# Kernel tuning notes

Hardware: AMD Instinct MI355X
Metric: run time of the kernel (lower is better)

Reference implementation:

```python
import jax, jax.numpy as jnp
import numpy as np

B, T, S, F, D, M = 8, 8192, 8192, 64, 64, 128
EPS = 1e-9


def _draw_omega(n_omega, d_feature, rng):
    # Stacked orthogonal blocks scaled by sqrt(d_feature), as in the TF module.
    n_blocks = (n_omega + d_feature - 1) // d_feature + 1
    blocks = []
    for _ in range(n_blocks):
        g = rng.standard_normal((d_feature, d_feature)).astype(np.float32)
        q, _ = np.linalg.qr(g)
        blocks.append(q * np.sqrt(float(d_feature)))
    return jnp.asarray(np.concatenate(blocks, axis=0)[:n_omega])


def setup_inputs() -> dict:
    k0 = jax.random.key(0)
    kq, kv, kk = jax.random.split(k0, 3)
    query = jax.random.normal(kq, (B, T, F), dtype=jnp.float32)
    value = jax.random.normal(kv, (B, S, D), dtype=jnp.float32)
    key = jax.random.normal(kk, (B, S, F), dtype=jnp.float32)
    omega = _draw_omega(M, F, np.random.default_rng(0))  # (M, F)
    return {"query": query, "value": value, "key": key, "omega": omega}


def _phi(x, omega):
    # x: (B, L, F) -> (B, L, 2M) positive random features
    m = omega.shape[0]
    square_sum = jnp.sum(x * x, axis=-1, keepdims=True) / 2.0  # (B, L, 1)
    xw = jnp.einsum('blf,mf->blm', x, omega)                   # (B, L, M)
    unnorm = jnp.exp(jnp.concatenate([xw, -xw], axis=-1) - square_sum) + EPS
    return unnorm / jnp.sqrt(2.0 * m)


def reference(query, value, key, omega):
    q = _phi(query, omega)  # (B, T, 2M)
    k = _phi(key, omega)    # (B, S, 2M)
    ones = jnp.ones(value.shape[:-1] + (1,), dtype=value.dtype)
    v1 = jnp.concatenate([value, ones], axis=-1)               # (B, S, D+1)
    kv = jnp.einsum('bsm,bsd->bmd', k, v1)                     # (B, 2M, D+1)
    qkv = jnp.einsum('btm,bmd->btd', q, kv)                    # (B, T, D+1)
    normalizer = qkv[:, :, -1:]
    return qkv[:, :, :-1] / normalizer
```

## Files before the change

kernel.cpp:

```cpp
#include <hip/hip_runtime.h>


constexpr int NB = 8;
constexpr int NT = 8192;
constexpr float EPSF = 1e-9f;
constexpr float SCALE = 0.0625f;

typedef short s8v __attribute__((ext_vector_type(8)));
typedef short s4v __attribute__((ext_vector_type(4)));
typedef float f4v __attribute__((ext_vector_type(4)));

__device__ inline f4v mfma16(s8v a, s8v b, f4v c) {
  return __builtin_amdgcn_mfma_f32_16x16x32_bf16(a, b, c, 0, 0, 0);
}

__device__ inline short bf16_rne(float f) {
  unsigned u = __builtin_bit_cast(unsigned, f);
  u += 0x7fffu + ((u >> 16) & 1u);
  return (short)(u >> 16);
}
__device__ inline float bf16_to_f(short h) {
  unsigned u = ((unsigned)(unsigned short)h) << 16;
  return __builtin_bit_cast(float, u);
}

__global__ void setup_omega(const float* __restrict__ omega,
                            short* __restrict__ ohf, short* __restrict__ olf) {
  int i = blockIdx.x * 256 + threadIdx.x;
  if (i >= 128 * 64) return;
  int jj = i & 7;
  int lane = (i >> 3) & 63;
  int h = (i >> 9) & 1;
  int ft = i >> 10;
  int m = ft * 16 + (lane & 15);
  int f = h * 32 + (lane >> 4) * 8 + jj;
  float wv = omega[m * 64 + f];
  short hh = bf16_rne(wv);
  ohf[i] = hh;
  olf[i] = bf16_rne(wv - bf16_to_f(hh));
}

struct PhiRows {
  s8v ah0, al0, ah1, al1;
  float ssr[4];
  float ss;
};

__device__ inline void split8(f4v a, f4v b, s8v& h, s8v& l) {
  float v[8] = {a.x, a.y, a.z, a.w, b.x, b.y, b.z, b.w};
#pragma unroll
  for (int j = 0; j < 8; ++j) {
    short hh = bf16_rne(v[j]);
    h[j] = hh;
    l[j] = bf16_rne(v[j] - bf16_to_f(hh));
  }
}

__device__ inline void load_phi_rows(const float* __restrict__ xrow_base, int lane, PhiRows& P) {
  const int r = lane & 15, q = lane >> 4;
  const float* p = xrow_base + r * 64 + q * 8;
  f4v u0 = *(const f4v*)(p);
  f4v u1 = *(const f4v*)(p + 4);
  f4v u2 = *(const f4v*)(p + 32);
  f4v u3 = *(const f4v*)(p + 36);
  float ss = u0.x * u0.x + u0.y * u0.y + u0.z * u0.z + u0.w * u0.w
           + u1.x * u1.x + u1.y * u1.y + u1.z * u1.z + u1.w * u1.w
           + u2.x * u2.x + u2.y * u2.y + u2.z * u2.z + u2.w * u2.w
           + u3.x * u3.x + u3.y * u3.y + u3.z * u3.z + u3.w * u3.w;
  ss += __shfl_xor(ss, 16, 64);
  ss += __shfl_xor(ss, 32, 64);
  ss *= 0.5f;
  P.ss = ss;
#pragma unroll
  for (int reg = 0; reg < 4; ++reg) P.ssr[reg] = __shfl(ss, q * 4 + reg, 64);
  split8(u0, u1, P.ah0, P.al0);
  split8(u2, u3, P.ah1, P.al1);
}

__device__ inline f4v phi_xw_tile(const PhiRows& P, const short* __restrict__ ohf,
                                  const short* __restrict__ olf, int ft, int lane) {
  const int o0 = ft * 1024 + lane * 8;
  s8v bh0 = *(const s8v*)(ohf + o0);
  s8v bh1 = *(const s8v*)(ohf + o0 + 512);
  s8v bl0 = *(const s8v*)(olf + o0);
  s8v bl1 = *(const s8v*)(olf + o0 + 512);
  f4v c = {0.f, 0.f, 0.f, 0.f};
  c = mfma16(P.ah0, bh0, c);
  c = mfma16(P.ah1, bh1, c);
  c = mfma16(P.al0, bh0, c);
  c = mfma16(P.al1, bh1, c);
  c = mfma16(P.ah0, bl0, c);
  c = mfma16(P.ah1, bl1, c);
  return c;
}

__device__ inline f4v phi_xw_tile_T(const PhiRows& P, const short* __restrict__ ohf,
                                    const short* __restrict__ olf, int ft, int lane) {
  const int o0 = ft * 1024 + lane * 8;
  s8v ah0 = *(const s8v*)(ohf + o0);
  s8v ah1 = *(const s8v*)(ohf + o0 + 512);
  s8v al0 = *(const s8v*)(olf + o0);
  s8v al1 = *(const s8v*)(olf + o0 + 512);
  f4v c = {0.f, 0.f, 0.f, 0.f};
  c = mfma16(ah0, P.ah0, c);
  c = mfma16(ah1, P.ah1, c);
  c = mfma16(al0, P.ah0, c);
  c = mfma16(al1, P.ah1, c);
  c = mfma16(ah0, P.al0, c);
  c = mfma16(ah1, P.al1, c);
  return c;
}

constexpr int KF_P = 72;
constexpr int QF_P = 264;
constexpr int PART_P = 72;
constexpr int PART_SZ = 256 * PART_P;

__global__ __launch_bounds__(256, 2) void kv_fused(
    const float* __restrict__ key, const float* __restrict__ value,
    const short* __restrict__ ohf, const short* __restrict__ olf,
    short* __restrict__ partial, float* __restrict__ kvacc, int use_partial) {
  __shared__ short kft[4 * 64 * KF_P];
  const int tid = threadIdx.x, lane = tid & 63, w = tid >> 6;
  const int b = blockIdx.x >> 6;
  const int s0 = (blockIdx.x & 63) * 128;
  const int q = lane >> 4, r15 = lane & 15;
  const int sign = w >> 1, th = w & 1;
  short* kw = kft + w * 64 * KF_P;

  s8v vone;
#pragma unroll
  for (int jj = 0; jj < 8; ++jj) vone[jj] = (r15 == 0) ? (short)0x3F80 : (short)0;

  f4v acc[4][5];
#pragma unroll
  for (int j = 0; j < 4; ++j)
#pragma unroll
    for (int n = 0; n < 5; ++n) acc[j][n] = f4v{0.f, 0.f, 0.f, 0.f};

  for (int sc = 0; sc < 2; ++sc) {
    const int sbase = s0 + sc * 64;
#pragma unroll
    for (int rg = 0; rg < 4; ++rg) {
      PhiRows P;
      load_phi_rows(key + ((size_t)b * NT + sbase + rg * 16) * 64, lane, P);
#pragma unroll
      for (int j = 0; j < 4; ++j) {
        f4v c = phi_xw_tile(P, ohf, olf, th * 4 + j, lane);
        s4v pk;
#pragma unroll
        for (int reg = 0; reg < 4; ++reg) {
          float xw = c[reg];
          float arg = sign ? (-xw - P.ssr[reg]) : (xw - P.ssr[reg]);
          pk[reg] = bf16_rne((__expf(arg) + EPSF) * SCALE);
        }
        *(s4v*)(kw + (j * 16 + r15) * KF_P + rg * 16 + q * 4) = pk;
      }
    }
    const float* vb = value + ((size_t)b * NT + sbase) * 64;
#pragma unroll
    for (int ks = 0; ks < 2; ++ks) {
      s8v bf[5];
#pragma unroll
      for (int n = 0; n < 4; ++n) {
#pragma unroll
        for (int jj = 0; jj < 8; ++jj)
          bf[n][jj] = bf16_rne(vb[(ks * 32 + q * 8 + jj) * 64 + n * 16 + r15]);
      }
      bf[4] = vone;
#pragma unroll
      for (int j = 0; j < 4; ++j) {
        s8v a = *(const s8v*)(kw + (j * 16 + r15) * KF_P + ks * 32 + q * 8);
#pragma unroll
        for (int n = 0; n < 5; ++n) acc[j][n] = mfma16(a, bf[n], acc[j][n]);
      }
    }
  }
  if (use_partial) {
#pragma unroll
    for (int j = 0; j < 4; ++j) {
#pragma unroll
      for (int n = 0; n < 4; ++n) {
#pragma unroll
        for (int reg = 0; reg < 4; ++reg)
          kw[(j * 16 + q * 4 + reg) * KF_P + n * 16 + r15] = bf16_rne(acc[j][n][reg]);
      }
      if (r15 == 0) {
#pragma unroll
        for (int reg = 0; reg < 4; ++reg)
          kw[(j * 16 + q * 4 + reg) * KF_P + 64] = bf16_rne(acc[j][4][reg]);
      }
    }
    short* pb = partial + (size_t)blockIdx.x * PART_SZ + w * 64 * PART_P;
#pragma unroll
    for (int i = 0; i < 9; ++i) {
      int e = i * 64 + lane;
      *(s8v*)(pb + e * 8) = *(const s8v*)(kw + e * 8);
    }
  } else {
    float* pb = kvacc + (size_t)b * PART_SZ;
#pragma unroll
    for (int j = 0; j < 4; ++j) {
      int m = w * 64 + j * 16 + q * 4;
#pragma unroll
      for (int n = 0; n < 4; ++n) {
        int d = n * 16 + r15;
#pragma unroll
        for (int reg = 0; reg < 4; ++reg)
          atomicAdd(pb + (size_t)(m + reg) * PART_P + d, acc[j][n][reg]);
      }
      if (r15 == 0)
#pragma unroll
        for (int reg = 0; reg < 4; ++reg)
          atomicAdd(pb + (size_t)(m + reg) * PART_P + 64, acc[j][4][reg]);
    }
  }
}

__global__ __launch_bounds__(256) void kv_finalize(
    const short* __restrict__ partial, const float* __restrict__ kvacc,
    short* __restrict__ kvfrag, int use_partial) {
  int i = blockIdx.x * 256 + threadIdx.x;
  int b = i / 20480;
  int rem = i - b * 20480;
  int m = rem / 80;
  int d = rem - m * 80;
  float s = 0.f;
  if (d < 65) {
    if (use_partial) {
      const short* p = partial + (size_t)(b * 64) * PART_SZ + m * PART_P + d;
#pragma unroll 8
      for (int c = 0; c < 64; ++c) s += bf16_to_f(p[(size_t)c * PART_SZ]);
    } else {
      s = kvacc[(size_t)b * PART_SZ + (size_t)m * PART_P + d];
    }
  }
  int ks = m >> 5, qq = (m >> 3) & 3, j = m & 7;
  int n = d >> 4, r = d & 15;
  int lane = qq * 16 + r;
  if (d < 80)
    kvfrag[(((size_t)b * 40 + ks * 5 + n) * 64 + lane) * 8 + j] = bf16_rne(s);
}

__global__ __launch_bounds__(256, 4) void qkv_fused(
    const float* __restrict__ query, const short* __restrict__ ohf,
    const short* __restrict__ olf, const short* __restrict__ kvfrag,
    float* __restrict__ out) {
  __shared__ __align__(16) short qf[64 * QF_P];
  const int tid = threadIdx.x, lane = tid & 63, w = tid >> 6;
  const int b = blockIdx.x >> 7;
  const int t0 = (blockIdx.x & 127) * 64;
  const int q = lane >> 4, r15 = lane & 15;

  {
    PhiRows P;
    load_phi_rows(query + ((size_t)b * NT + t0 + w * 16) * 64, lane, P);
    const int t_loc = w * 16 + r15;
#pragma unroll
    for (int ft = 0; ft < 8; ++ft) {
      f4v c = phi_xw_tile_T(P, ohf, olf, ft, lane);
      s4v pk, nk;
#pragma unroll
      for (int reg = 0; reg < 4; ++reg) {
        float xw = c[reg];
        pk[reg] = bf16_rne((__expf(xw - P.ss) + EPSF) * SCALE);
        nk[reg] = bf16_rne((__expf(-xw - P.ss) + EPSF) * SCALE);
      }
      *(s4v*)(qf + t_loc * QF_P + ft * 16 + q * 4) = pk;
      *(s4v*)(qf + t_loc * QF_P + 128 + ft * 16 + q * 4) = nk;
    }
  }
  f4v acc[5];
#pragma unroll
  for (int n = 0; n < 5; ++n) acc[n] = f4v{0.f, 0.f, 0.f, 0.f};
  const short* kvb = kvfrag + (size_t)b * 40 * 512;
#pragma unroll
  for (int ks = 0; ks < 8; ++ks) {
    s8v a = *(const s8v*)(qf + (w * 16 + r15) * QF_P + ks * 32 + q * 8);
#pragma unroll
    for (int n = 0; n < 5; ++n) {
      s8v bf = *(const s8v*)(kvb + ((size_t)(ks * 5 + n)) * 512 + lane * 8);
      acc[n] = mfma16(a, bf, acc[n]);
    }
  }
  float den_r[4];
#pragma unroll
  for (int reg = 0; reg < 4; ++reg) den_r[reg] = __shfl(acc[4][reg], lane & 48, 64);
  float* stg = (float*)(qf + w * 16 * QF_P);
#pragma unroll
  for (int n = 0; n < 4; ++n)
#pragma unroll
    for (int reg = 0; reg < 4; ++reg) {
      int row = q * 4 + reg;
      int col = n * 16 + r15;
      stg[row * 68 + col] = acc[n][reg] / den_r[reg];
    }
  float* ob = out + ((size_t)b * NT + t0 + w * 16) * 64;
#pragma unroll
  for (int rr = 0; rr < 4; ++rr) {
    int row = rr * 4 + q;
    int c4 = r15 * 4;
    *(f4v*)(ob + row * 64 + c4) = *(const f4v*)(stg + row * 68 + c4);
  }
}

extern "C" void kernel_launch(void* const* d_in, const int* in_sizes, int n_in,
                              void* d_out, int out_size, void* d_ws, size_t ws_size,
                              hipStream_t stream) {
  const float* query = (const float*)d_in[0];
  const float* value = (const float*)d_in[1];
  const float* key   = (const float*)d_in[2];
  const float* omega = (const float*)d_in[3];
  float* out = (float*)d_out;

  char* ws = (char*)d_ws;
  short* ohf = (short*)ws;
  short* olf = (short*)(ws + 16384);
  short* kvfrag = (short*)(ws + 32768);
  short* partial = (short*)(ws + 360448);
  float* kvacc = (float*)(ws + 360448);
  const size_t need_full = 360448 + (size_t)512 * PART_SZ * 2;
  const int use_partial = (ws_size >= need_full) ? 1 : 0;

  setup_omega<<<32, 256, 0, stream>>>(omega, ohf, olf);
  if (!use_partial) {
    hipMemsetAsync(kvacc, 0, (size_t)8 * PART_SZ * 4, stream);
  }
  kv_fused<<<512, 256, 0, stream>>>(key, value, ohf, olf, partial, kvacc, use_partial);
  kv_finalize<<<640, 256, 0, stream>>>(partial, kvacc, kvfrag, use_partial);
  qkv_fused<<<1024, 256, 0, stream>>>(query, ohf, olf, kvfrag, out);
}
```

Before: 130.3 us.

## Split kv_fused into 64-row chunks with paired positive/negative features per wave

The kv_fused kernel now runs twice as many blocks, each covering 64 key rows instead of looping over two 64-row chunks. Each wave computes both the positive and negative exponential features for its own omega tiles, which shares each xw result across both signs. Launch bounds rise to four blocks per CU. In exchange the partial buffer doubles in size, so kv_finalize has to reduce 128 partials per batch with a remapped feature index, which adds reduction traffic and raises the workspace requirement.

```diff
diff --git a/kernel.cpp b/kernel.cpp
--- a/kernel.cpp
+++ b/kernel.cpp
@@ -115,80 +115,77 @@
 constexpr int QF_P = 264;
 constexpr int PART_P = 72;
 constexpr int PART_SZ = 256 * PART_P;
-
-__global__ __launch_bounds__(256, 2) void kv_fused(
+constexpr int KV_GRID = 1024;
+
+__global__ __launch_bounds__(256, 4) void kv_fused(
     const float* __restrict__ key, const float* __restrict__ value,
     const short* __restrict__ ohf, const short* __restrict__ olf,
     short* __restrict__ partial, float* __restrict__ kvacc, int use_partial) {
   __shared__ short kft[4 * 64 * KF_P];
   const int tid = threadIdx.x, lane = tid & 63, w = tid >> 6;
-  const int b = blockIdx.x >> 6;
-  const int s0 = (blockIdx.x & 63) * 128;
+  const int b = blockIdx.x >> 7;
+  const int s0 = (blockIdx.x & 127) * 64;
   const int q = lane >> 4, r15 = lane & 15;
-  const int sign = w >> 1, th = w & 1;
   short* kw = kft + w * 64 * KF_P;
 
   s8v vone;
 #pragma unroll
   for (int jj = 0; jj < 8; ++jj) vone[jj] = (r15 == 0) ? (short)0x3F80 : (short)0;
 
+#pragma unroll
+  for (int rg = 0; rg < 4; ++rg) {
+    PhiRows P;
+    load_phi_rows(key + ((size_t)b * NT + s0 + rg * 16) * 64, lane, P);
+#pragma unroll
+    for (int ftl = 0; ftl < 2; ++ftl) {
+      f4v c = phi_xw_tile(P, ohf, olf, w * 2 + ftl, lane);
+      s4v pk, nk;
+#pragma unroll
+      for (int reg = 0; reg < 4; ++reg) {
+        float xw = c[reg];
+        pk[reg] = bf16_rne((__expf(xw - P.ssr[reg]) + EPSF) * SCALE);
+        nk[reg] = bf16_rne((__expf(-xw - P.ssr[reg]) + EPSF) * SCALE);
+      }
+      *(s4v*)(kw + (ftl * 16 + r15) * KF_P + rg * 16 + q * 4) = pk;
+      *(s4v*)(kw + (32 + ftl * 16 + r15) * KF_P + rg * 16 + q * 4) = nk;
+    }
+  }
   f4v acc[4][5];
 #pragma unroll
-  for (int j = 0; j < 4; ++j)
-#pragma unroll
-    for (int n = 0; n < 5; ++n) acc[j][n] = f4v{0.f, 0.f, 0.f, 0.f};
-
-  for (int sc = 0; sc < 2; ++sc) {
-    const int sbase = s0 + sc * 64;
-#pragma unroll
-    for (int rg = 0; rg < 4; ++rg) {
-      PhiRows P;
-      load_phi_rows(key + ((size_t)b * NT + sbase + rg * 16) * 64, lane, P);
-#pragma unroll
-      for (int j = 0; j < 4; ++j) {
-        f4v c = phi_xw_tile(P, ohf, olf, th * 4 + j, lane);
-        s4v pk;
-#pragma unroll
-        for (int reg = 0; reg < 4; ++reg) {
-          float xw = c[reg];
-          float arg = sign ? (-xw - P.ssr[reg]) : (xw - P.ssr[reg]);
-          pk[reg] = bf16_rne((__expf(arg) + EPSF) * SCALE);
-        }
-        *(s4v*)(kw + (j * 16 + r15) * KF_P + rg * 16 + q * 4) = pk;
-      }
-    }
-    const float* vb = value + ((size_t)b * NT + sbase) * 64;
-#pragma unroll
-    for (int ks = 0; ks < 2; ++ks) {
-      s8v bf[5];
+  for (int mt = 0; mt < 4; ++mt)
+#pragma unroll
+    for (int n = 0; n < 5; ++n) acc[mt][n] = f4v{0.f, 0.f, 0.f, 0.f};
+  const float* vb = value + ((size_t)b * NT + s0) * 64;
+#pragma unroll
+  for (int ks = 0; ks < 2; ++ks) {
+    s8v bf[5];
+#pragma unroll
+    for (int n = 0; n < 4; ++n) {
+#pragma unroll
+      for (int jj = 0; jj < 8; ++jj)
+        bf[n][jj] = bf16_rne(vb[(ks * 32 + q * 8 + jj) * 64 + n * 16 + r15]);
+    }
+    bf[4] = vone;
+#pragma unroll
+    for (int mt = 0; mt < 4; ++mt) {
+      s8v a = *(const s8v*)(kw + (mt * 16 + r15) * KF_P + ks * 32 + q * 8);
+#pragma unroll
+      for (int n = 0; n < 5; ++n) acc[mt][n] = mfma16(a, bf[n], acc[mt][n]);
+    }
+  }
+  if (use_partial) {
+#pragma unroll
+    for (int mt = 0; mt < 4; ++mt) {
 #pragma unroll
       for (int n = 0; n < 4; ++n) {
 #pragma unroll
-        for (int jj = 0; jj < 8; ++jj)
-          bf[n][jj] = bf16_rne(vb[(ks * 32 + q * 8 + jj) * 64 + n * 16 + r15]);
-      }
-      bf[4] = vone;
-#pragma unroll
-      for (int j = 0; j < 4; ++j) {
-        s8v a = *(const s8v*)(kw + (j * 16 + r15) * KF_P + ks * 32 + q * 8);
-#pragma unroll
-        for (int n = 0; n < 5; ++n) acc[j][n] = mfma16(a, bf[n], acc[j][n]);
-      }
-    }
-  }
-  if (use_partial) {
-#pragma unroll
-    for (int j = 0; j < 4; ++j) {
-#pragma unroll
-      for (int n = 0; n < 4; ++n) {
-#pragma unroll
         for (int reg = 0; reg < 4; ++reg)
-          kw[(j * 16 + q * 4 + reg) * KF_P + n * 16 + r15] = bf16_rne(acc[j][n][reg]);
+          kw[(mt * 16 + q * 4 + reg) * KF_P + n * 16 + r15] = bf16_rne(acc[mt][n][reg]);
       }
       if (r15 == 0) {
 #pragma unroll
         for (int reg = 0; reg < 4; ++reg)
-          kw[(j * 16 + q * 4 + reg) * KF_P + 64] = bf16_rne(acc[j][4][reg]);
+          kw[(mt * 16 + q * 4 + reg) * KF_P + 64] = bf16_rne(acc[mt][4][reg]);
       }
     }
     short* pb = partial + (size_t)blockIdx.x * PART_SZ + w * 64 * PART_P;
@@ -200,19 +197,16 @@
   } else {
     float* pb = kvacc + (size_t)b * PART_SZ;
 #pragma unroll
-    for (int j = 0; j < 4; ++j) {
-      int m = w * 64 + j * 16 + q * 4;
-#pragma unroll
-      for (int n = 0; n < 4; ++n) {
-        int d = n * 16 + r15;
-#pragma unroll
-        for (int reg = 0; reg < 4; ++reg)
-          atomicAdd(pb + (size_t)(m + reg) * PART_P + d, acc[j][n][reg]);
-      }
-      if (r15 == 0)
-#pragma unroll
-        for (int reg = 0; reg < 4; ++reg)
-          atomicAdd(pb + (size_t)(m + reg) * PART_P + 64, acc[j][4][reg]);
+    for (int mt = 0; mt < 4; ++mt) {
+#pragma unroll
+      for (int reg = 0; reg < 4; ++reg) {
+        int ml = mt * 16 + q * 4 + reg;
+        int m = (ml < 32) ? (w * 32 + ml) : (128 + w * 32 + (ml - 32));
+#pragma unroll
+        for (int n = 0; n < 4; ++n)
+          atomicAdd(pb + (size_t)m * PART_P + n * 16 + r15, acc[mt][n][reg]);
+        if (r15 == 0) atomicAdd(pb + (size_t)m * PART_P + 64, acc[mt][4][reg]);
+      }
     }
   }
 }
@@ -228,9 +222,13 @@
   float s = 0.f;
   if (d < 65) {
     if (use_partial) {
-      const short* p = partial + (size_t)(b * 64) * PART_SZ + m * PART_P + d;
+      int w_, ml;
+      if (m < 128) { w_ = m >> 5; ml = m & 31; }
+      else { int mm = m - 128; w_ = mm >> 5; ml = 32 + (mm & 31); }
+      int pr = w_ * 64 + ml;
+      const short* p = partial + (size_t)(b * 128) * PART_SZ + pr * PART_P + d;
 #pragma unroll 8
-      for (int c = 0; c < 64; ++c) s += bf16_to_f(p[(size_t)c * PART_SZ]);
+      for (int c = 0; c < 128; ++c) s += bf16_to_f(p[(size_t)c * PART_SZ]);
     } else {
       s = kvacc[(size_t)b * PART_SZ + (size_t)m * PART_P + d];
     }
@@ -319,14 +317,14 @@
   short* kvfrag = (short*)(ws + 32768);
   short* partial = (short*)(ws + 360448);
   float* kvacc = (float*)(ws + 360448);
-  const size_t need_full = 360448 + (size_t)512 * PART_SZ * 2;
+  const size_t need_full = 360448 + (size_t)KV_GRID * PART_SZ * 2;
   const int use_partial = (ws_size >= need_full) ? 1 : 0;
 
   setup_omega<<<32, 256, 0, stream>>>(omega, ohf, olf);
   if (!use_partial) {
     hipMemsetAsync(kvacc, 0, (size_t)8 * PART_SZ * 4, stream);
   }
-  kv_fused<<<512, 256, 0, stream>>>(key, value, ohf, olf, partial, kvacc, use_partial);
+  kv_fused<<<KV_GRID, 256, 0, stream>>>(key, value, ohf, olf, partial, kvacc, use_partial);
   kv_finalize<<<640, 256, 0, stream>>>(partial, kvacc, kvfrag, use_partial);
   qkv_fused<<<1024, 256, 0, stream>>>(query, ohf, olf, kvfrag, out);
 }
```

After: 135.0 us. 3.6% more time.
